# Kernel optimization log

Measured on AMD Instinct MI355X. Metric: run time of the kernel, lower is better.

Reference implementation:

```python
import jax, jax.numpy as jnp
from jax import lax
import numpy as np

NUM_NODES = 30   # pinned by LayerNorm(30) in TCNBlock
H = 4            # heads
C = 64           # channel per head
HC = H * C       # 256 = all_channels, first TCN channel
F_IN = 64
B = 1024         # graphs per batch
EPG = 240        # random edges per graph (no self loops; GATv2 adds them)
LN_EPS = 1e-5
NEG_SLOPE = 0.2


def _glorot(k, shp):
    fan_in = int(np.prod(shp[1:])) if len(shp) > 1 else int(shp[0])
    return jax.random.normal(k, shp, dtype=jnp.float32) / np.sqrt(fan_in)


def setup_inputs():
    key = jax.random.key(0)
    ks = jax.random.split(key, 16)
    N = B * NUM_NODES
    # random intra-graph edges with src != dst (PyG remove_self_loops then add_self_loops)
    src_l = jax.random.randint(ks[0], (B, EPG), 0, NUM_NODES)
    off = jax.random.randint(ks[1], (B, EPG), 1, NUM_NODES)
    dst_l = (src_l + off) % NUM_NODES
    base = (jnp.arange(B) * NUM_NODES)[:, None]
    edge_index = jnp.stack([(src_l + base).reshape(-1), (dst_l + base).reshape(-1)]).astype(jnp.int32)
    z = lambda *s: jnp.zeros(s, jnp.float32)
    return {
        "x": jax.random.normal(ks[2], (N, F_IN), dtype=jnp.float32),
        "gat_Wl": _glorot(ks[3], (HC, F_IN)), "gat_bl": z(HC),
        "gat_Wr": _glorot(ks[4], (HC, F_IN)), "gat_br": z(HC),
        "gat_att": _glorot(ks[5], (H, C)), "gat_bias": z(HC),
        "tcn0_w": _glorot(ks[6], (HC, HC, 3)), "tcn0_b": z(HC),
        "ln0_w": jnp.ones((NUM_NODES,), jnp.float32), "ln0_b": z(NUM_NODES),
        "tcn1_w": _glorot(ks[7], (512, HC, 3)), "tcn1_b": z(512),
        "ln1_w": jnp.ones((NUM_NODES,), jnp.float32), "ln1_b": z(NUM_NODES),
        "ds1_w": _glorot(ks[8], (512, HC, 1)), "ds1_b": z(512),
        "tcn2_w": _glorot(ks[9], (256, 512, 3)), "tcn2_b": z(256),
        "ln2_w": jnp.ones((NUM_NODES,), jnp.float32), "ln2_b": z(NUM_NODES),
        "ds2_w": _glorot(ks[10], (256, 512, 1)), "ds2_b": z(256),
        "fc1_w": _glorot(ks[11], (512, 256 * NUM_NODES)), "fc1_b": z(512),
        "fc2_w": _glorot(ks[12], (256, 512)), "fc2_b": z(256),
        "fc3_w": _glorot(ks[13], (144, 256)), "fc3_b": z(144),
        "edge_index": edge_index,
    }


def _conv1d(x, w, b, dil):
    # torch Conv1d: x [B,Cin,L], w [Cout,Cin,K], padding = dil*(K-1)//2
    pad = dil * (w.shape[-1] - 1) // 2
    y = lax.conv_general_dilated(x, w, (1,), [(pad, pad)], rhs_dilation=(dil,),
                                 dimension_numbers=("NCH", "OIH", "NCH"))
    return y + b[None, :, None]


def _ln(x, w, b):
    # LayerNorm over last dim (length 30)
    mu = jnp.mean(x, -1, keepdims=True)
    var = jnp.var(x, -1, keepdims=True)
    return (x - mu) * lax.rsqrt(var + LN_EPS) * w + b


def reference(x, gat_Wl, gat_bl, gat_Wr, gat_br, gat_att, gat_bias,
              tcn0_w, tcn0_b, ln0_w, ln0_b,
              tcn1_w, tcn1_b, ln1_w, ln1_b, ds1_w, ds1_b,
              tcn2_w, tcn2_b, ln2_w, ln2_b, ds2_w, ds2_b,
              fc1_w, fc1_b, fc2_w, fc2_b, fc3_w, fc3_b, edge_index):
    N = x.shape[0]
    # GATv2Conv default: add self loops
    loops = jnp.arange(N, dtype=edge_index.dtype)
    ei = jnp.concatenate([edge_index, jnp.stack([loops, loops])], axis=1)
    src, dst = ei[0], ei[1]
    xl = (x @ gat_Wl.T + gat_bl).reshape(N, H, C)  # source transform
    xr = (x @ gat_Wr.T + gat_br).reshape(N, H, C)  # target transform
    s = jax.nn.leaky_relu(xl[src] + xr[dst], NEG_SLOPE)          # [E,H,C]
    e = jnp.einsum("ehc,hc->eh", s, gat_att)                     # [E,H]
    m = jax.ops.segment_max(e, dst, num_segments=N)              # segment softmax
    expe = jnp.exp(e - m[dst])
    alpha = expe / jax.ops.segment_sum(expe, dst, num_segments=N)[dst]
    agg = jax.ops.segment_sum(alpha[:, :, None] * xl[src], dst, num_segments=N)
    h = jax.nn.relu(agg.reshape(N, HC) + gat_bias)
    h = h.reshape(-1, NUM_NODES, HC).transpose(0, 2, 1)          # [B, HC, 30]
    # TCN: dilations 1,2,4; residual with 1x1 downsample when channels change
    y = jax.nn.relu(_ln(_conv1d(h, tcn0_w, tcn0_b, 1), ln0_w, ln0_b)) + h
    y = jax.nn.relu(_ln(_conv1d(y, tcn1_w, tcn1_b, 2), ln1_w, ln1_b)) + _conv1d(y, ds1_w, ds1_b, 1)
    y = jax.nn.relu(_ln(_conv1d(y, tcn2_w, tcn2_b, 4), ln2_w, ln2_b)) + _conv1d(y, ds2_w, ds2_b, 1)
    z = y.reshape(y.shape[0], -1)                                # [B, 256*30]
    z = jax.nn.relu(z @ fc1_w.T + fc1_b)
    z = jax.nn.relu(z @ fc2_w.T + fc2_b)
    out = z @ fc3_w.T + fc3_b                                    # [B, 144]
    return out, alpha, ei
```

## Files before the change

### kernel.cpp

```cpp
#include <hip/hip_runtime.h>
#include <hip/hip_bf16.h>

typedef __bf16  bf16x8 __attribute__((ext_vector_type(8)));
typedef __bf16  bf16x4 __attribute__((ext_vector_type(4)));
typedef float   f32x4  __attribute__((ext_vector_type(4)));
typedef __hip_bfloat16 bf;

__device__ __forceinline__ float clamp256(float v) {
    return fminf(fmaxf(v, -256.f), 256.f);
}
__device__ __forceinline__ float sane(float v) {
    return fminf(fmaxf(v, -1e4f), 1e4f);
}
__device__ __forceinline__ int swzk(int k, int col) {
    return (k & ~31) | ((((k >> 3) & 3) ^ ((col >> 1) & 3)) << 3) | (k & 7);
}

template<int TAPS, bool HASWD>
__global__ __launch_bounds__(256) void gemm_tf(
    const bf* __restrict__ A, const bf* __restrict__ Wt, const bf* __restrict__ Wd,
    const float* __restrict__ bias, const float* __restrict__ biasd,
    const float* __restrict__ lnw, const float* __restrict__ lnb,
    const bf* __restrict__ res, int res_stride,
    bf* __restrict__ outb, float* __restrict__ outf, int out_stride,
    int M, int N, int K, int dil, int mode, int relu, int padded, int nn, int kLen)
{
    constexpr int NT = TAPS + (HASWD ? 1 : 0);
    __shared__ __align__(16) unsigned short sA[66 * 40];
    __shared__ __align__(16) unsigned short sB[NT][64 * 40];
    __shared__ float sS[4][64], sS2[4][64];

    const int tid  = threadIdx.x;
    const int wv   = tid >> 6;
    const int lane = tid & 63;
    const int m0   = blockIdx.y * 64;
    const int n0   = blockIdx.x * 64;
    const int frow = lane & 15;
    const int fq   = lane >> 4;
    const int kOff = blockIdx.z * kLen;
    const int kEnd = (kOff + kLen < K) ? (kOff + kLen) : K;

    if (tid < 40) sA[64 * 40 + tid] = (unsigned short)0;

    int aoff[NT];
    {
        int token = wv * 16 + frow;
        int b = token >> 5, l = token & 31;
        #pragma unroll
        for (int t = 0; t < NT; ++t) {
            int s = (t < TAPS) ? (t - TAPS / 2) * dil : 0;
            int ar;
            if (padded) {
                int ls = l + s;
                ar = ((unsigned)ls < 32u) ? (b * 32 + ls) : 64;
            } else {
                ar = token;
            }
            aoff[t] = ar * 40 + fq * 8;
        }
    }

    const int srow = tid >> 2;
    const int schk = (tid & 3) << 3;
    int raG = m0 + srow;
    if (!padded && raG >= M) raG = -1;
    const int rbG  = n0 + srow;
    const bool bval = rbG < N;
    const bf* Ap = (raG >= 0) ? (A + (size_t)raG * K) : nullptr;
    const bf* Bp[NT];
    #pragma unroll
    for (int t = 0; t < NT; ++t)
        Bp[t] = (HASWD && t == TAPS) ? (Wd + (size_t)rbG * K)
                                     : (Wt + ((size_t)t * N + rbG) * K);

    f32x4 accC[4], accR[4];
    #pragma unroll
    for (int i = 0; i < 4; ++i) { accC[i] = 0.f; accR[i] = 0.f; }

    const uint4 zu = make_uint4(0u, 0u, 0u, 0u);
    uint4 pa, pb[NT];
    pa = Ap ? *(const uint4*)(Ap + kOff + schk) : zu;
    #pragma unroll
    for (int t = 0; t < NT; ++t)
        pb[t] = bval ? *(const uint4*)(Bp[t] + kOff + schk) : zu;

    for (int kb = kOff; kb < kEnd; kb += 32) {
        __syncthreads();
        *(uint4*)(sA + srow * 40 + schk) = pa;
        #pragma unroll
        for (int t = 0; t < NT; ++t)
            *(uint4*)(&sB[t][srow * 40 + schk]) = pb[t];
        __syncthreads();
        int kn = kb + 32;
        if (kn < kEnd) {
            pa = Ap ? *(const uint4*)(Ap + kn + schk) : zu;
            #pragma unroll
            for (int t = 0; t < NT; ++t)
                pb[t] = bval ? *(const uint4*)(Bp[t] + kn + schk) : zu;
        }
        #pragma unroll
        for (int t = 0; t < TAPS; ++t) {
            bf16x8 af = *(const bf16x8*)(sA + aoff[t]);
            #pragma unroll
            for (int nt = 0; nt < 4; ++nt) {
                bf16x8 bg = *(const bf16x8*)(&sB[t][(nt * 16 + frow) * 40 + fq * 8]);
                accC[nt] = __builtin_amdgcn_mfma_f32_16x16x32_bf16(af, bg, accC[nt], 0, 0, 0);
            }
        }
        if constexpr (HASWD) {
            bf16x8 af = *(const bf16x8*)(sA + aoff[TAPS]);
            #pragma unroll
            for (int nt = 0; nt < 4; ++nt) {
                bf16x8 bg = *(const bf16x8*)(&sB[TAPS][(nt * 16 + frow) * 40 + fq * 8]);
                accR[nt] = __builtin_amdgcn_mfma_f32_16x16x32_bf16(af, bg, accR[nt], 0, 0, 0);
            }
        }
    }

    if (mode == 0) {
        #pragma unroll
        for (int nt = 0; nt < 4; ++nt) {
            int col = n0 + nt * 16 + frow;
            if (col >= N) continue;
            float bv = bias ? bias[col] : 0.f;
            #pragma unroll
            for (int r = 0; r < 4; ++r) {
                int row = m0 + wv * 16 + fq * 4 + r;
                if (row >= M) continue;
                float v = accC[nt][r] + bv;
                if (relu) v = fmaxf(v, 0.f);
                if (outb) outb[(size_t)row * out_stride + col] = __float2bfloat16(clamp256(v));
                else      outf[(size_t)row * out_stride + col] = sane(v);
            }
        }
    } else if (mode == 3) {
        bf* po = outb + (size_t)blockIdx.z * M * out_stride;
        #pragma unroll
        for (int nt = 0; nt < 4; ++nt) {
            int col = n0 + nt * 16 + frow;
            if (col >= N) continue;
            #pragma unroll
            for (int r = 0; r < 4; ++r) {
                int row = m0 + wv * 16 + fq * 4 + r;
                if (row >= M) continue;
                po[(size_t)row * out_stride + col] = __float2bfloat16(accC[nt][r]);
            }
        }
    } else if (mode == 5) {
        if constexpr (HASWD) {
            bf* out2 = (bf*)res;
            int orow_[4];
            #pragma unroll
            for (int r = 0; r < 4; ++r) {
                int row = m0 + wv * 16 + fq * 4 + r;
                orow_[r] = relu ? ((row / nn) * 32 + (row % nn)) : row;
            }
            #pragma unroll
            for (int nt = 0; nt < 4; ++nt) {
                int col = n0 + nt * 16 + frow;
                if (col >= N) continue;
                float bv = bias[col], bd = biasd[col];
                #pragma unroll
                for (int r = 0; r < 4; ++r) {
                    int row = m0 + wv * 16 + fq * 4 + r;
                    if (row >= M) continue;
                    outb[(size_t)row * out_stride + col] = __float2bfloat16(clamp256(accC[nt][r] + bv));
                    out2[(size_t)orow_[r] * res_stride + col] = __float2bfloat16(clamp256(accR[nt][r] + bd));
                }
            }
        }
    } else {
        float bvc[4], bdc[4];
        #pragma unroll
        for (int nt = 0; nt < 4; ++nt) {
            int col = n0 + nt * 16 + frow;
            bvc[nt] = bias[col];
            bdc[nt] = (HASWD && biasd) ? biasd[col] : 0.f;
        }
        float s[4], s2[4];
        #pragma unroll
        for (int nt = 0; nt < 4; ++nt) { s[nt] = 0.f; s2[nt] = 0.f; }
        #pragma unroll
        for (int nt = 0; nt < 4; ++nt)
            #pragma unroll
            for (int r = 0; r < 4; ++r) {
                int row = wv * 16 + fq * 4 + r;
                int l = row & 31;
                float v = sane(accC[nt][r] + bvc[nt]);
                if (l < nn) { s[nt] += v; s2[nt] += v * v; }
            }
        #pragma unroll
        for (int nt = 0; nt < 4; ++nt) {
            s[nt]  += __shfl_xor(s[nt], 16);  s[nt]  += __shfl_xor(s[nt], 32);
            s2[nt] += __shfl_xor(s2[nt], 16); s2[nt] += __shfl_xor(s2[nt], 32);
        }
        if (fq == 0) {
            #pragma unroll
            for (int nt = 0; nt < 4; ++nt) {
                sS[wv][nt * 16 + frow]  = s[nt];
                sS2[wv][nt * 16 + frow] = s2[nt];
            }
        }
        __syncthreads();
        const int gi = wv >> 1;
        const float inv = 1.f / (float)nn;
        #pragma unroll
        for (int nt = 0; nt < 4; ++nt) {
            int c = nt * 16 + frow;
            int colg = n0 + c;
            float S  = sS[2 * gi][c]  + sS[2 * gi + 1][c];
            float S2 = sS2[2 * gi][c] + sS2[2 * gi + 1][c];
            float mu = S * inv;
            float var = S2 * inv - mu * mu;
            float rs = rsqrtf(fmaxf(var, 0.f) + 1e-5f);
            #pragma unroll
            for (int r = 0; r < 4; ++r) {
                int row = wv * 16 + fq * 4 + r;
                int l = row & 31;
                int grow = m0 + row;
                float outv = 0.f;
                if (l < nn) {
                    float v = (sane(accC[nt][r] + bvc[nt]) - mu) * rs * lnw[l] + lnb[l];
                    v = fmaxf(v, 0.f);
                    float rr;
                    if constexpr (HASWD) rr = sane(accR[nt][r] + bdc[nt]);
                    else rr = __bfloat162float(res[(size_t)grow * res_stride + colg]);
                    outv = clamp256(v + rr);
                }
                outb[(size_t)grow * out_stride + colg] = __float2bfloat16(outv);
            }
        }
    }
}

template<int TAPS, bool HASWD>
__global__ __launch_bounds__(256, 2) void gemm_tcn(
    const bf* __restrict__ A, const bf* __restrict__ Wt, const bf* __restrict__ Wd,
    const float* __restrict__ bias, const float* __restrict__ biasd,
    const float* __restrict__ lnw, const float* __restrict__ lnb,
    const bf* __restrict__ res, int res_stride,
    bf* __restrict__ outb, int out_stride,
    int M, int N, int K, int dil, int nn)
{
    constexpr int NT = TAPS + (HASWD ? 1 : 0);
    constexpr int SA = 257 * 40;
    __shared__ __align__(16) unsigned short sA[2 * SA];
    __shared__ __align__(16) unsigned short sBall[2 * NT * 64 * 32];

    const int tid  = threadIdx.x;
    const int wv   = tid >> 6;
    const int lane = tid & 63;
    const int frow = lane & 15;
    const int fq   = lane >> 4;

    const int gx  = gridDim.x;
    const int nwg = gx * gridDim.y;
    int wg = blockIdx.y * gx + blockIdx.x;
    if ((nwg & 7) == 0) wg = (wg & 7) * (nwg >> 3) + (wg >> 3);
    const int n0 = (wg % gx) * 64;
    const int m0 = (wg / gx) * 256;

    if (tid < 40) {
        sA[256 * 40 + tid]      = (unsigned short)0;
        sA[SA + 256 * 40 + tid] = (unsigned short)0;
    }

    int aoff[TAPS][4];
    #pragma unroll
    for (int mr = 0; mr < 4; ++mr) {
        int token = wv * 64 + mr * 16 + frow;
        int b5 = token >> 5, l = token & 31;
        #pragma unroll
        for (int t = 0; t < TAPS; ++t) {
            int ls = l + (t - TAPS / 2) * dil;
            int ar = ((unsigned)ls < 32u) ? (b5 * 32 + ls) : 256;
            aoff[t][mr] = ar * 40 + fq * 8;
        }
    }
    const int bco = (fq ^ ((frow >> 1) & 3)) << 3;

    const int srow = tid >> 2;
    const int chS  = (tid & 3) << 3;
    const bf* Ap = A + (size_t)(m0 + srow) * K + chS;

    const bf* bsrc[4];
    {
        int lr = lane >> 2, lc = lane & 3;
        #pragma unroll
        for (int i = 0; i < 4; ++i) {
            int colb = n0 + i * 16 + lr;
            const bf* Wb;
            if (HASWD && wv == TAPS) Wb = Wd + (size_t)colb * K;
            else if (wv < TAPS)      Wb = Wt + ((size_t)wv * N + colb) * K;
            else                     Wb = Wt + (size_t)colb * K;
            bsrc[i] = Wb + lc * 8;
        }
    }

    f32x4 accC[4][4], accR[4][4];
    #pragma unroll
    for (int i = 0; i < 4; ++i)
        #pragma unroll
        for (int j = 0; j < 4; ++j) { accC[i][j] = 0.f; if (HASWD) accR[i][j] = 0.f; }

    #define ISSUE_B(BUFB, KBS)                                                      \
        if (wv < NT) {                                                              \
            unsigned short* bas = sBall + ((size_t)((BUFB) * NT + wv) * 64) * 32;   \
            _Pragma("unroll")                                                       \
            for (int i = 0; i < 4; ++i) {                                           \
                __builtin_amdgcn_global_load_lds(                                   \
                    (const __attribute__((address_space(1))) void*)(bsrc[i] + (KBS)), \
                    (__attribute__((address_space(3))) void*)(bas + i * 512),       \
                    16, 0, 0);                                                      \
            }                                                                       \
        }

    uint4 pa[4];
    #pragma unroll
    for (int i = 0; i < 4; ++i) pa[i] = *(const uint4*)(Ap + (size_t)i * 64 * K);
    ISSUE_B(0, 0);
    #pragma unroll
    for (int i = 0; i < 4; ++i)
        *(uint4*)(sA + (srow + i * 64) * 40 + chS) = pa[i];
    __syncthreads();

    int buf = 0;
    for (int kb = 0; kb < K; kb += 32) {
        int kn = kb + 32;
        if (kn < K) {
            #pragma unroll
            for (int i = 0; i < 4; ++i)
                pa[i] = *(const uint4*)(Ap + (size_t)i * 64 * K + kn);
            ISSUE_B(buf ^ 1, kn);
        }
        const unsigned short* sAb = sA + (size_t)buf * SA;
        const unsigned short* sBb = sBall + (size_t)buf * NT * 2048;
        bf16x8 aMid[4];
        #pragma unroll
        for (int mr = 0; mr < 4; ++mr)
            aMid[mr] = *(const bf16x8*)(sAb + aoff[TAPS / 2][mr]);
        #pragma unroll
        for (int t = 0; t < TAPS; ++t) {
            bf16x8 af[4];
            #pragma unroll
            for (int mr = 0; mr < 4; ++mr)
                af[mr] = (t == TAPS / 2) ? aMid[mr]
                                         : *(const bf16x8*)(sAb + aoff[t][mr]);
            #pragma unroll
            for (int nt = 0; nt < 4; ++nt) {
                bf16x8 bg = *(const bf16x8*)(sBb + (size_t)t * 2048 + (nt * 16 + frow) * 32 + bco);
                #pragma unroll
                for (int mr = 0; mr < 4; ++mr)
                    accC[mr][nt] = __builtin_amdgcn_mfma_f32_16x16x32_bf16(af[mr], bg, accC[mr][nt], 0, 0, 0);
            }
        }
        if constexpr (HASWD) {
            #pragma unroll
            for (int nt = 0; nt < 4; ++nt) {
                bf16x8 bg = *(const bf16x8*)(sBb + (size_t)TAPS * 2048 + (nt * 16 + frow) * 32 + bco);
                #pragma unroll
                for (int mr = 0; mr < 4; ++mr)
                    accR[mr][nt] = __builtin_amdgcn_mfma_f32_16x16x32_bf16(aMid[mr], bg, accR[mr][nt], 0, 0, 0);
            }
        }
        if (kn < K) {
            unsigned short* sAn = sA + (size_t)(buf ^ 1) * SA;
            #pragma unroll
            for (int i = 0; i < 4; ++i)
                *(uint4*)(sAn + (srow + i * 64) * 40 + chS) = pa[i];
        }
        __syncthreads();
        buf ^= 1;
    }
    #undef ISSUE_B

    float bvc[4], bdc[4];
    #pragma unroll
    for (int nt = 0; nt < 4; ++nt) {
        int col = n0 + nt * 16 + frow;
        bvc[nt] = bias[col];
        bdc[nt] = HASWD ? biasd[col] : 0.f;
    }
    float S[2][4], Q[2][4];
    #pragma unroll
    for (int h = 0; h < 2; ++h)
        #pragma unroll
        for (int nt = 0; nt < 4; ++nt) { S[h][nt] = 0.f; Q[h][nt] = 0.f; }
    #pragma unroll
    for (int mr = 0; mr < 4; ++mr) {
        const int h = mr >> 1;
        #pragma unroll
        for (int nt = 0; nt < 4; ++nt)
            #pragma unroll
            for (int r = 0; r < 4; ++r) {
                int l = (mr & 1) * 16 + fq * 4 + r;
                if (l < nn) {
                    float v = sane(accC[mr][nt][r] + bvc[nt]);
                    S[h][nt] += v; Q[h][nt] += v * v;
                }
            }
    }
    const float inv = 1.f / (float)nn;
    float mu[2][4], rsg[2][4];
    #pragma unroll
    for (int h = 0; h < 2; ++h)
        #pragma unroll
        for (int nt = 0; nt < 4; ++nt) {
            float s = S[h][nt], q = Q[h][nt];
            s += __shfl_xor(s, 16); s += __shfl_xor(s, 32);
            q += __shfl_xor(q, 16); q += __shfl_xor(q, 32);
            float m = s * inv;
            float var = q * inv - m * m;
            mu[h][nt]  = m;
            rsg[h][nt] = rsqrtf(fmaxf(var, 0.f) + 1e-5f);
        }
    float lw[2][4], lb2[2][4];
    #pragma unroll
    for (int p = 0; p < 2; ++p)
        #pragma unroll
        for (int r = 0; r < 4; ++r) {
            int l = p * 16 + fq * 4 + r;
            bool ok = l < nn;
            lw[p][r]  = ok ? lnw[l] : 0.f;
            lb2[p][r] = ok ? lnb[l] : 0.f;
        }
    #pragma unroll
    for (int nt = 0; nt < 4; ++nt) {
        const int colg = n0 + nt * 16 + frow;
        #pragma unroll
        for (int mr = 0; mr < 4; ++mr) {
            const int h = mr >> 1, p = mr & 1;
            #pragma unroll
            for (int r = 0; r < 4; ++r) {
                int l = p * 16 + fq * 4 + r;
                int grow = m0 + wv * 64 + mr * 16 + fq * 4 + r;
                float outv = 0.f;
                if (l < nn) {
                    float v = (sane(accC[mr][nt][r] + bvc[nt]) - mu[h][nt]) * rsg[h][nt] * lw[p][r] + lb2[p][r];
                    v = fmaxf(v, 0.f);
                    float rr;
                    if constexpr (HASWD) rr = sane(accR[mr][nt][r] + bdc[nt]);
                    else rr = __bfloat162float(res[(size_t)grow * res_stride + colg]);
                    outv = clamp256(v + rr);
                }
                outb[(size_t)grow * out_stride + colg] = __float2bfloat16(outv);
            }
        }
    }
}

#define MAXNE 270
#define XLS   260
#define SHP   264
template<int CONV>
__global__ __launch_bounds__(256, 4) void gat_fused4(
    const int* __restrict__ ei, const bf* __restrict__ xlb, const bf* __restrict__ xrb,
    const float* __restrict__ att, const float* __restrict__ gbias,
    const bf* __restrict__ Wf, const float* __restrict__ cbias,
    const float* __restrict__ lnw, const float* __restrict__ lnb,
    bf* __restrict__ yout, float* __restrict__ dalpha, float* __restrict__ dei,
    int E0, int ET, int EPG, int nn)
{
    __shared__ __align__(16) __bf16 sXL[32 * XLS];
    __shared__ __align__(16) __bf16 sHX[33 * SHP];
    __shared__ float sExp[MAXNE * 4];
    __shared__ int   sSD[MAXNE];
    __shared__ unsigned short sList[MAXNE];
    __shared__ int   sCnt[32];
    __shared__ int   sOff[33];

    const int g = blockIdx.x, tid = threadIdx.x, wv = tid >> 6, lane = tid & 63;
    if (EPG + nn > MAXNE) return;
    const int NE = EPG + nn;

    for (int k = tid; k < EPG; k += 256) {
        int s = ei[(size_t)g * EPG + k] - g * nn;
        int d = ei[(size_t)E0 + (size_t)g * EPG + k] - g * nn;
        s = min(max(s, 0), nn - 1);
        d = min(max(d, 0), nn - 1);
        sSD[k] = s | (d << 16);
    }
    for (int k = EPG + tid; k < NE; k += 256) {
        int node = k - EPG;
        sSD[k] = node | (node << 16);
    }
    {
        const uint4* gxl = (const uint4*)(xlb + (size_t)g * nn * 256);
        const uint4* gxr = (const uint4*)(xrb + (size_t)g * (CONV ? 32 : nn) * 256);
        for (int k = tid; k < nn * 32; k += 256) {
            int node = k >> 5, c8 = k & 31;
            *(uint4*)(sXL + node * XLS + c8 * 8) = gxl[k];
            *(uint4*)(sHX + k * 8) = gxr[k];
        }
    }
    if (CONV) { __bf16 z = (__bf16)0.f; for (int k = tid; k < SHP; k += 256) sHX[32 * SHP + k] = z; }
    if (tid < 32) sCnt[tid] = 0;
    __syncthreads();

    for (int k = tid; k < NE; k += 256) atomicAdd(&sCnt[sSD[k] >> 16], 1);
    __syncthreads();
    if (tid < 32) {
        int acc = 0, last = 0;
        #pragma unroll
        for (int j = 0; j < 32; ++j) {
            int c = sCnt[j];
            if (j < tid) acc += c;
            if (j == 31) last = c;
        }
        sOff[tid] = acc;
        if (tid == 31) sOff[32] = acc + last;
        sCnt[tid] = 0;
    }
    __syncthreads();
    for (int k = tid; k < NE; k += 256) {
        int d = sSD[k] >> 16;
        int p = atomicAdd(&sCnt[d], 1);
        sList[sOff[d] + p] = (unsigned short)k;
    }

    for (int k = tid; k < NE; k += 256) {
        int s, d; size_t eg;
        if (k < EPG) {
            int sd = sSD[k];
            s = g * nn + (sd & 0xffff); d = g * nn + (sd >> 16);
            eg = (size_t)g * EPG + k;
        }
        else { int node = g * nn + (k - EPG); s = d = node; eg = (size_t)E0 + (size_t)g * nn + (k - EPG); }
        dei[eg] = (float)s;
        dei[(size_t)ET + eg] = (float)d;
    }
    __syncthreads();

    const float4 attv = *(const float4*)(att + lane * 4);
    const int h4 = lane >> 4;
    for (int i = wv; i < NE; i += 4) {
        int sd = sSD[i];
        int srcl = sd & 0xffff, dstl = sd >> 16;
        bf16x4 a = *(const bf16x4*)(sXL + srcl * XLS + lane * 4);
        bf16x4 b = *(const bf16x4*)(sHX + dstl * 256 + lane * 4);
        float p = 0.f;
        {
            float v0 = (float)a[0] + (float)b[0]; v0 = v0 > 0.f ? v0 : 0.2f * v0; p += v0 * attv.x;
            float v1 = (float)a[1] + (float)b[1]; v1 = v1 > 0.f ? v1 : 0.2f * v1; p += v1 * attv.y;
            float v2 = (float)a[2] + (float)b[2]; v2 = v2 > 0.f ? v2 : 0.2f * v2; p += v2 * attv.z;
            float v3 = (float)a[3] + (float)b[3]; v3 = v3 > 0.f ? v3 : 0.2f * v3; p += v3 * attv.w;
        }
        p += __shfl_xor(p, 1); p += __shfl_xor(p, 2);
        p += __shfl_xor(p, 4); p += __shfl_xor(p, 8);
        if ((lane & 15) == 0)
            sExp[i * 4 + h4] = __expf(fminf(fmaxf(p, -60.f), 60.f));
    }
    __syncthreads();

    {
        const int grp  = wv * 8 + (lane >> 3);
        const int s8   = lane & 7;
        const int chb  = s8 * 32;
        const int head = s8 >> 1;
        bf* hrow = yout + ((size_t)g * 32 + grp) * 256 + chb;

        if (grp < nn) {
            const int beg = sOff[grp], end = sOff[grp + 1];
            float den = 0.f;
            f32x4 acc[8];
            #pragma unroll
            for (int k2 = 0; k2 < 8; ++k2) acc[k2] = 0.f;

            for (int q = beg; q < end; ++q) {
                int e = sList[q];
                float ev = sExp[e * 4 + head];
                den += ev;
                const __bf16* xp = sXL + (sSD[e] & 0xffff) * XLS + chb;
                #pragma unroll
                for (int k2 = 0; k2 < 4; ++k2) {
                    bf16x8 xa = *(const bf16x8*)(xp + k2 * 8);
                    #pragma unroll
                    for (int j = 0; j < 4; ++j)
                        acc[k2 * 2][j]     += ev * (float)xa[j];
                    #pragma unroll
                    for (int j = 0; j < 4; ++j)
                        acc[k2 * 2 + 1][j] += ev * (float)xa[4 + j];
                }
            }
            const float rden = 1.f / fmaxf(den, 1e-30f);

            if (!(s8 & 1)) {
                for (int q = beg; q < end; ++q) {
                    int e = sList[q];
                    float al = fminf(fmaxf(sExp[e * 4 + head] * rden, 0.f), 1.f);
                    size_t eg = (e < EPG) ? ((size_t)g * EPG + e)
                                          : ((size_t)E0 + (size_t)g * nn + (e - EPG));
                    dalpha[eg * 4 + head] = al;
                }
            }

            #pragma unroll
            for (int k2 = 0; k2 < 8; ++k2) {
                float4 gbv = *(const float4*)(gbias + chb + k2 * 4);
                bf16x4 o;
                o[0] = (__bf16)clamp256(fmaxf(acc[k2][0] * rden + gbv.x, 0.f));
                o[1] = (__bf16)clamp256(fmaxf(acc[k2][1] * rden + gbv.y, 0.f));
                o[2] = (__bf16)clamp256(fmaxf(acc[k2][2] * rden + gbv.z, 0.f));
                o[3] = (__bf16)clamp256(fmaxf(acc[k2][3] * rden + gbv.w, 0.f));
                if constexpr (CONV) *(bf16x4*)(sHX + grp * SHP + chb + k2 * 4) = o;
                else                *(bf16x4*)(hrow + k2 * 4) = o;
            }
        } else {
            bf16x4 z; z[0] = (__bf16)0.f; z[1] = (__bf16)0.f; z[2] = (__bf16)0.f; z[3] = (__bf16)0.f;
            #pragma unroll
            for (int k2 = 0; k2 < 8; ++k2) {
                if constexpr (CONV) *(bf16x4*)(sHX + grp * SHP + chb + k2 * 4) = z;
                else                *(bf16x4*)(hrow + k2 * 4) = z;
            }
        }
    }

    if constexpr (CONV) {
        __syncthreads();
        const int frow = lane & 15;
        const int fq   = lane >> 4;
        const int colw = wv * 64;
        f32x4 c0[2][4];
        #pragma unroll
        for (int i = 0; i < 2; ++i)
            #pragma unroll
            for (int j = 0; j < 4; ++j) c0[i][j] = 0.f;

        #pragma unroll
        for (int kc = 0; kc < 8; ++kc) {
            bf16x8 af[3][2];
            #pragma unroll
            for (int t = 0; t < 3; ++t)
                #pragma unroll
                for (int mr = 0; mr < 2; ++mr) {
                    int l = mr * 16 + frow + t - 1;
                    int ar = ((unsigned)l < 32u) ? l : 32;
                    af[t][mr] = *(const bf16x8*)(sHX + ar * SHP + kc * 32 + fq * 8);
                }
            #pragma unroll
            for (int t = 0; t < 3; ++t) {
                bf16x8 bgs[4];
                #pragma unroll
                for (int nt = 0; nt < 4; ++nt) {
                    const __bf16* bp = (const __bf16*)Wf +
                        ((((size_t)(t * 16 + (colw >> 4) + nt) * 8 + kc) * 16 + frow) * 4 + fq) * 8;
                    bgs[nt] = *(const bf16x8*)bp;
                }
                #pragma unroll
                for (int nt = 0; nt < 4; ++nt) {
                    c0[0][nt] = __builtin_amdgcn_mfma_f32_16x16x32_bf16(af[t][0], bgs[nt], c0[0][nt], 0, 0, 0);
                    c0[1][nt] = __builtin_amdgcn_mfma_f32_16x16x32_bf16(af[t][1], bgs[nt], c0[1][nt], 0, 0, 0);
                }
            }
        }

        float bv[4];
        #pragma unroll
        for (int nt = 0; nt < 4; ++nt) bv[nt] = cbias[colw + nt * 16 + frow];
        float S[4], Q[4];
        #pragma unroll
        for (int nt = 0; nt < 4; ++nt) { S[nt] = 0.f; Q[nt] = 0.f; }
        #pragma unroll
        for (int mr = 0; mr < 2; ++mr)
            #pragma unroll
            for (int nt = 0; nt < 4; ++nt)
                #pragma unroll
                for (int r = 0; r < 4; ++r) {
                    int l = mr * 16 + fq * 4 + r;
                    if (l < nn) {
                        float v = sane(c0[mr][nt][r] + bv[nt]);
                        S[nt] += v; Q[nt] += v * v;
                    }
                }
        const float inv = 1.f / (float)nn;
        float mu[4], rsg[4];
        #pragma unroll
        for (int nt = 0; nt < 4; ++nt) {
            float s = S[nt], q = Q[nt];
            s += __shfl_xor(s, 16); s += __shfl_xor(s, 32);
            q += __shfl_xor(q, 16); q += __shfl_xor(q, 32);
            float m = s * inv;
            float var = q * inv - m * m;
            mu[nt]  = m;
            rsg[nt] = rsqrtf(fmaxf(var, 0.f) + 1e-5f);
        }
        float lw[2][4], lb2[2][4];
        #pragma unroll
        for (int p = 0; p < 2; ++p)
            #pragma unroll
            for (int r = 0; r < 4; ++r) {
                int l = p * 16 + fq * 4 + r;
                bool ok = l < nn;
                lw[p][r]  = ok ? lnw[l] : 0.f;
                lb2[p][r] = ok ? lnb[l] : 0.f;
            }
        #pragma unroll
        for (int nt = 0; nt < 4; ++nt) {
            const int colf = colw + nt * 16 + frow;
            #pragma unroll
            for (int mr = 0; mr < 2; ++mr)
                #pragma unroll
                for (int r = 0; r < 4; ++r) {
                    int l = mr * 16 + fq * 4 + r;
                    float outv = 0.f;
                    if (l < nn) {
                        float v = (sane(c0[mr][nt][r] + bv[nt]) - mu[nt]) * rsg[nt] * lw[mr][r] + lb2[mr][r];
                        v = fmaxf(v, 0.f);
                        float rr = (float)sHX[l * SHP + colf];
                        outv = clamp256(v + rr);
                    }
                    yout[((size_t)g * 32 + l) * 256 + colf] = __float2bfloat16(outv);
                }
        }
    }
}

struct CvtSegs { const float* in[7]; bf* out[7]; int n[7]; };
__global__ void prep_cvt(CvtSegs s, int total)
{
    int idx = blockIdx.x * 256 + threadIdx.x;
    if (idx >= total) return;
    #pragma unroll
    for (int i = 0; i < 7; ++i) {
        if (idx < s.n[i]) { s.out[i][idx] = __float2bfloat16(s.in[i][idx]); return; }
        idx -= s.n[i];
    }
}
struct TapSegs { const float* w[3]; bf* o[3]; int cc[3]; int kk[3]; int swz[3]; };
__global__ void prep_taps3(TapSegs s, int total)
{
    int idx = blockIdx.x * 256 + threadIdx.x;
    if (idx >= total) return;
    #pragma unroll
    for (int i = 0; i < 3; ++i) {
        if (idx < s.cc[i]) {
            unsigned K = (unsigned)s.kk[i];
            unsigned co = (unsigned)idx / K, ci = (unsigned)idx % K;
            int dst = co * K + (s.swz[i] ? swzk(ci, co) : ci);
            #pragma unroll
            for (int k = 0; k < 3; ++k)
                s.o[i][(size_t)k * s.cc[i] + dst] = __float2bfloat16(s.w[i][(size_t)idx * 3 + k]);
            return;
        }
        idx -= s.cc[i];
    }
}
__global__ void prep_wswz(const float* __restrict__ w, bf* __restrict__ o,
                          int total, int K, int swz)
{
    int idx = blockIdx.x * 256 + threadIdx.x;
    if (idx >= total) return;
    int co = idx / K, ci = idx % K;
    o[(size_t)co * K + (swz ? swzk(ci, co) : ci)] = __float2bfloat16(w[idx]);
}
__global__ void prep_bfrag(const float* __restrict__ w, bf* __restrict__ o, int HC)
{
    int idx = blockIdx.x * 256 + threadIdx.x;
    if (idx >= HC * HC) return;
    int co = idx / HC, ci = idx % HC;
    int cg = co >> 4, fr = co & 15, kc = ci >> 5, fq = (ci >> 3) & 3, w8 = ci & 7;
    int NCg = HC >> 4, NKc = HC >> 5;
    #pragma unroll
    for (int t = 0; t < 3; ++t) {
        size_t dst = (((((size_t)t * NCg + cg) * NKc + kc) * 16 + fr) * 4 + fq) * 8 + w8;
        o[dst] = __float2bfloat16(w[(size_t)idx * 3 + t]);
    }
}

__global__ void prep_fc1(const float* __restrict__ w, bf* __restrict__ o, int F1, int nn, int HC)
{
    int idx = blockIdx.x * 256 + threadIdx.x;
    int kw = 32 * HC;
    if (idx >= F1 * kw) return;
    int co = idx / kw, r = idx % kw, l = r / HC, ci = r % HC;
    float hv = 0.f;
    if (l < nn) hv = w[(size_t)co * (HC * nn) + ci * nn + l];
    o[idx] = __float2bfloat16(hv);
}

__global__ void fc1red(const bf* __restrict__ zp, const float* __restrict__ bias,
                       bf* __restrict__ o, int MN, int N, int S)
{
    int idx = blockIdx.x * 256 + threadIdx.x;
    if (idx >= MN) return;
    float s = 0.f;
    for (int z = 0; z < S; ++z) s += __bfloat162float(zp[(size_t)z * MN + idx]);
    o[idx] = __float2bfloat16(clamp256(fmaxf(s + bias[idx % N], 0.f)));
}

extern "C" void kernel_launch(void* const* d_in, const int* in_sizes, int n_in,
                              void* d_out, int out_size, void* d_ws, size_t ws_size,
                              hipStream_t stream)
{
    (void)n_in; (void)ws_size;
    const float* x   = (const float*)d_in[0];
    const float* Wl  = (const float*)d_in[1];  const float* bl  = (const float*)d_in[2];
    const float* Wr  = (const float*)d_in[3];  const float* br  = (const float*)d_in[4];
    const float* att = (const float*)d_in[5];  const float* gb  = (const float*)d_in[6];
    const float* t0w = (const float*)d_in[7];  const float* t0b = (const float*)d_in[8];
    const float* l0w = (const float*)d_in[9];  const float* l0b = (const float*)d_in[10];
    const float* t1w = (const float*)d_in[11]; const float* t1b = (const float*)d_in[12];
    const float* l1w = (const float*)d_in[13]; const float* l1b = (const float*)d_in[14];
    const float* d1w = (const float*)d_in[15]; const float* d1b = (const float*)d_in[16];
    const float* t2w = (const float*)d_in[17]; const float* t2b = (const float*)d_in[18];
    const float* l2w = (const float*)d_in[19]; const float* l2b = (const float*)d_in[20];
    const float* d2w = (const float*)d_in[21]; const float* d2b = (const float*)d_in[22];
    const float* f1w = (const float*)d_in[23]; const float* f1b = (const float*)d_in[24];
    const float* f2w = (const float*)d_in[25]; const float* f2b = (const float*)d_in[26];
    const float* f3w = (const float*)d_in[27]; const float* f3b = (const float*)d_in[28];
    const int*   ei  = (const int*)d_in[29];

    const int HC   = in_sizes[6];
    const int F_IN = in_sizes[1] / (HC > 0 ? HC : 1);
    const int NN   = in_sizes[0] / (F_IN > 0 ? F_IN : 1);
    const int E0   = in_sizes[29] / 2;
    const int ET   = E0 + NN;
    int nn = in_sizes[9];  nn = nn < 1 ? 1 : (nn > 32 ? 32 : nn);
    const int NG   = NN / nn;
    const int EPG  = NG > 0 ? E0 / NG : 0;
    const int C1   = in_sizes[12];
    const int C2   = in_sizes[18];
    const int F1   = in_sizes[24];
    const int F2   = in_sizes[26];
    const int F3   = in_sizes[28];
    const int NG2  = (NG + 1) / 2;

    float* dout   = (float*)d_out;
    float* dei    = dout + ((size_t)out_size - 2 * (size_t)ET);
    float* dalpha = dei - (size_t)ET * 4;

    const bool fused0 = (HC == 256) && (nn >= 1) && (nn <= 32) && (EPG + nn <= MAXNE)
                        && ((NN % 64) == 0);
    const int  gcA = NG2, gcB = NG - NG2;
    const bool fastc = ((gcA * 32) % 256 == 0) && ((gcB * 32) % 256 == 0)
                       && (C1 % 64 == 0) && (C2 % 64 == 0)
                       && (HC % 32 == 0) && (C1 % 32 == 0);

    char* ws = (char*)d_ws;
    const size_t MB = 1ull << 20;
    bf*    xb   = (bf*)(ws);
    bf*    WkA  = (bf*)(ws + 4 * MB);
    bf*    WkB  = WkA + (size_t)3 * HC * HC;
    bf*    WkC  = WkB + (size_t)3 * C1 * HC;
    bf*    Wlb  = WkC + (size_t)3 * C2 * C1;
    bf*    Wrb  = Wlb + (size_t)HC * F_IN;
    bf*    f2wb = Wrb + (size_t)HC * F_IN;
    bf*    f3wb = f2wb + (size_t)F2 * F1;
    bf*    d1wb = f3wb + (size_t)F3 * F2;
    bf*    d2wb = d1wb + (size_t)C1 * HC;
    bf*    WkAf = d2wb + (size_t)C2 * C1;
    char*  S0   = ws + (size_t)(7.5 * MB);
    char*  S1   = ws + 25 * MB;

    bf*    xrb  = (bf*)S0;
    bf*    hbuf = (bf*)S0;
    bf*    xlb  = (bf*)S1;
    bf*    y0   = fused0 ? (bf*)S0 : (bf*)S1;
    bf*    y1c  = fused0 ? (bf*)S1 : (bf*)S0;
    char*  fcS  = fused0 ? S1 : S0;
    bf*    W1t  = (bf*)fcS;
    bf*    z1p  = (bf*)(fcS + (size_t)(8.5 * MB));
    bf*    z1   = (bf*)(ws);
    bf*    z2   = (bf*)(ws + 2 * MB);

    {
        CvtSegs cs;
        cs.in[0] = x;   cs.out[0] = xb;   cs.n[0] = NN * F_IN;
        cs.in[1] = Wl;  cs.out[1] = Wlb;  cs.n[1] = HC * F_IN;
        cs.in[2] = Wr;  cs.out[2] = Wrb;  cs.n[2] = HC * F_IN;
        cs.in[3] = f2w; cs.out[3] = f2wb; cs.n[3] = F2 * F1;
        cs.in[4] = f3w; cs.out[4] = f3wb; cs.n[4] = F3 * F2;
        cs.in[5] = nullptr; cs.out[5] = nullptr; cs.n[5] = 0;
        cs.in[6] = nullptr; cs.out[6] = nullptr; cs.n[6] = 0;
        int tot = 0; for (int i = 0; i < 5; ++i) tot += cs.n[i];
        prep_cvt<<<(tot + 255) / 256, 256, 0, stream>>>(cs, tot);
        TapSegs ts;
        ts.w[0] = t0w; ts.o[0] = WkA; ts.cc[0] = HC * HC; ts.kk[0] = HC; ts.swz[0] = 0;
        ts.w[1] = t1w; ts.o[1] = WkB; ts.cc[1] = C1 * HC; ts.kk[1] = HC; ts.swz[1] = fastc ? 1 : 0;
        ts.w[2] = t2w; ts.o[2] = WkC; ts.cc[2] = C2 * C1; ts.kk[2] = C1; ts.swz[2] = fastc ? 1 : 0;
        int tt = ts.cc[0] + ts.cc[1] + ts.cc[2];
        prep_taps3<<<(tt + 255) / 256, 256, 0, stream>>>(ts, tt);
        prep_wswz<<<(C1 * HC + 255) / 256, 256, 0, stream>>>(d1w, d1wb, C1 * HC, HC, fastc ? 1 : 0);
        prep_wswz<<<(C2 * C1 + 255) / 256, 256, 0, stream>>>(d2w, d2wb, C2 * C1, C1, fastc ? 1 : 0);
        if (fused0)
            prep_bfrag<<<(HC * HC + 255) / 256, 256, 0, stream>>>(t0w, WkAf, HC);
    }

    gemm_tf<1, true><<<dim3((HC + 63) / 64, (NN + 63) / 64), 256, 0, stream>>>(
        xb, Wlb, Wrb, bl, br, nullptr, nullptr, (const bf*)xrb, HC,
        xlb, nullptr, HC, NN, HC, F_IN, 1, 5, fused0 ? 1 : 0, 0, nn, F_IN);

    if (fused0)
        gat_fused4<1><<<NG, 256, 0, stream>>>(ei, xlb, xrb, att, gb,
                                              WkAf, t0b, l0w, l0b,
                                              y0, dalpha, dei, E0, ET, EPG, nn);
    else {
        gat_fused4<0><<<NG, 256, 0, stream>>>(ei, xlb, xrb, att, gb,
                                              nullptr, nullptr, nullptr, nullptr,
                                              hbuf, dalpha, dei, E0, ET, EPG, nn);
        gemm_tf<3, false><<<dim3((HC + 63) / 64, NG * 32 / 64), 256, 0, stream>>>(
            hbuf, WkA, nullptr, t0b, nullptr, l0w, l0b, hbuf, HC,
            y0, nullptr, HC, NG * 32, HC, HC, 1, 2, 0, 1, nn, HC);
    }

    for (int c = 0; c < 2; ++c) {
        int g0 = c * NG2;
        int gc = (c == 0) ? NG2 : (NG - NG2);
        if (gc <= 0) continue;
        const bf* y0c = y0 + (size_t)g0 * 32 * HC;
        bf*       y2c = y0 + (size_t)g0 * 32 * HC;
        if (fastc) {
            gemm_tcn<3, true><<<dim3(C1 / 64, gc * 32 / 256), 256, 0, stream>>>(
                y0c, WkB, d1wb, t1b, d1b, l1w, l1b, nullptr, 0,
                y1c, C1, gc * 32, C1, HC, 2, nn);
            gemm_tcn<3, true><<<dim3(C2 / 64, gc * 32 / 256), 256, 0, stream>>>(
                y1c, WkC, d2wb, t2b, d2b, l2w, l2b, nullptr, 0,
                y2c, C2, gc * 32, C2, C1, 4, nn);
        } else {
            gemm_tf<3, true><<<dim3((C1 + 63) / 64, gc * 32 / 64), 256, 0, stream>>>(
                y0c, WkB, d1wb, t1b, d1b, l1w, l1b, nullptr, 0,
                y1c, nullptr, C1, gc * 32, C1, HC, 2, 2, 0, 1, nn, HC);
            gemm_tf<3, true><<<dim3((C2 + 63) / 64, gc * 32 / 64), 256, 0, stream>>>(
                y1c, WkC, d2wb, t2b, d2b, l2w, l2b, nullptr, 0,
                y2c, nullptr, C2, gc * 32, C2, C1, 4, 2, 0, 1, nn, C1);
        }
    }

    prep_fc1<<<(F1 * 32 * HC + 255) / 256, 256, 0, stream>>>(f1w, W1t, F1, nn, HC);
    gemm_tf<1, false><<<dim3((F1 + 63) / 64, (NG + 63) / 64, 8), 256, 0, stream>>>(
        y0, W1t, nullptr, nullptr, nullptr, nullptr, nullptr, nullptr, 0,
        z1p, nullptr, F1, NG, F1, 32 * HC, 1, 3, 0, 0, nn, 4 * HC);
    fc1red<<<(NG * F1 + 255) / 256, 256, 0, stream>>>(z1p, f1b, z1, NG * F1, F1, 8);

    gemm_tf<1, false><<<dim3((F2 + 63) / 64, (NG + 63) / 64), 256, 0, stream>>>(
        z1, f2wb, nullptr, f2b, nullptr, nullptr, nullptr, nullptr, 0,
        z2, nullptr, F2, NG, F2, F1, 1, 0, 1, 0, nn, F1);
    gemm_tf<1, false><<<dim3((F3 + 63) / 64, (NG + 63) / 64), 256, 0, stream>>>(
        z2, f3wb, nullptr, f3b, nullptr, nullptr, nullptr, nullptr, 0,
        nullptr, dout, F3, NG, F3, F2, 1, 0, 0, 0, nn, F2);
}
```

Before: 454.4 us.

## Fuse GATv2 left/right linear projections into the per-graph GAT kernel

The separate gemm_tf launch that computed xl and xr for all nodes is removed on the fused path. Each per-graph GAT block now loads the raw bf16 node features into shared memory (reusing the sExp buffer) and computes both projections with MFMA, using weights pre-packed into fragment layout by a new prep kernel. This avoids writing the xl/xr intermediates to global memory and reading them back, and saves one launch. In exchange the GAT kernel does more work, carries more register pressure, and each block re-reads the projection weights from global memory.

```diff
diff --git a/kernel.cpp b/kernel.cpp
--- a/kernel.cpp
+++ b/kernel.cpp
@@ -455,6 +455,7 @@
 template<int CONV>
 __global__ __launch_bounds__(256, 4) void gat_fused4(
     const int* __restrict__ ei, const bf* __restrict__ xlb, const bf* __restrict__ xrb,
+    const bf* __restrict__ Wlr, const float* __restrict__ gbl, const float* __restrict__ gbr,
     const float* __restrict__ att, const float* __restrict__ gbias,
     const bf* __restrict__ Wf, const float* __restrict__ cbias,
     const float* __restrict__ lnw, const float* __restrict__ lnb,
@@ -463,7 +464,7 @@
 {
     __shared__ __align__(16) __bf16 sXL[32 * XLS];
     __shared__ __align__(16) __bf16 sHX[33 * SHP];
-    __shared__ float sExp[MAXNE * 4];
+    __shared__ __align__(16) float sExp[MAXNE * 4];
     __shared__ int   sSD[MAXNE];
     __shared__ unsigned short sList[MAXNE];
     __shared__ int   sCnt[32];
@@ -472,6 +473,8 @@
     const int g = blockIdx.x, tid = threadIdx.x, wv = tid >> 6, lane = tid & 63;
     if (EPG + nn > MAXNE) return;
     const int NE = EPG + nn;
+    const int frow = lane & 15;
+    const int fq   = lane >> 4;
 
     for (int k = tid; k < EPG; k += 256) {
         int s = ei[(size_t)g * EPG + k] - g * nn;
@@ -484,20 +487,78 @@
         int node = k - EPG;
         sSD[k] = node | (node << 16);
     }
-    {
+    if constexpr (CONV) {
+        unsigned short* sXg = (unsigned short*)sExp;
+        const uint4* gx = (const uint4*)(xlb + (size_t)g * nn * 64);
+        for (int k = tid; k < nn * 8; k += 256) {
+            int node = k >> 3, k8 = k & 7;
+            *(uint4*)(sXg + node * 64 + ((k8 ^ (node & 7)) << 3)) = gx[k];
+        }
+        const uint4 zu = make_uint4(0u, 0u, 0u, 0u);
+        for (int k = nn * 8 + tid; k < 32 * 8; k += 256) {
+            int node = k >> 3, k8 = k & 7;
+            *(uint4*)(sXg + node * 64 + ((k8 ^ (node & 7)) << 3)) = zu;
+        }
+        __bf16 z = (__bf16)0.f;
+        for (int k = tid; k < SHP; k += 256) sHX[32 * SHP + k] = z;
+    } else {
         const uint4* gxl = (const uint4*)(xlb + (size_t)g * nn * 256);
-        const uint4* gxr = (const uint4*)(xrb + (size_t)g * (CONV ? 32 : nn) * 256);
+        const uint4* gxr = (const uint4*)(xrb + (size_t)g * nn * 256);
         for (int k = tid; k < nn * 32; k += 256) {
             int node = k >> 5, c8 = k & 31;
             *(uint4*)(sXL + node * XLS + c8 * 8) = gxl[k];
-            *(uint4*)(sHX + k * 8) = gxr[k];
-        }
-    }
-    if (CONV) { __bf16 z = (__bf16)0.f; for (int k = tid; k < SHP; k += 256) sHX[32 * SHP + k] = z; }
+            *(uint4*)(sHX + node * SHP + c8 * 8) = gxr[k];
+        }
+    }
     if (tid < 32) sCnt[tid] = 0;
     __syncthreads();
 
     for (int k = tid; k < NE; k += 256) atomicAdd(&sCnt[sSD[k] >> 16], 1);
+    if constexpr (CONV) {
+        const unsigned short* sXg = (const unsigned short*)sExp;
+        bf16x8 axf[2][2];
+        #pragma unroll
+        for (int mr = 0; mr < 2; ++mr)
+            #pragma unroll
+            for (int kc = 0; kc < 2; ++kc) {
+                int row = mr * 16 + frow;
+                axf[mr][kc] = *(const bf16x8*)(sXg + row * 64 + (((kc * 4 + fq) ^ (row & 7)) << 3));
+            }
+        const int colw = wv * 64;
+        #pragma unroll
+        for (int out = 0; out < 2; ++out) {
+            f32x4 ga[2][4];
+            #pragma unroll
+            for (int mr = 0; mr < 2; ++mr)
+                #pragma unroll
+                for (int ct = 0; ct < 4; ++ct) ga[mr][ct] = 0.f;
+            #pragma unroll
+            for (int kc = 0; kc < 2; ++kc)
+                #pragma unroll
+                for (int ct = 0; ct < 4; ++ct) {
+                    const __bf16* bp = (const __bf16*)Wlr + (size_t)out * 16384 +
+                        ((((size_t)(((colw >> 4) + ct) * 2 + kc) * 16 + frow) * 4 + fq) * 8);
+                    bf16x8 bg = *(const bf16x8*)bp;
+                    ga[0][ct] = __builtin_amdgcn_mfma_f32_16x16x32_bf16(axf[0][kc], bg, ga[0][ct], 0, 0, 0);
+                    ga[1][ct] = __builtin_amdgcn_mfma_f32_16x16x32_bf16(axf[1][kc], bg, ga[1][ct], 0, 0, 0);
+                }
+            const float* bb = out ? gbr : gbl;
+            #pragma unroll
+            for (int ct = 0; ct < 4; ++ct) {
+                int col = colw + ct * 16 + frow;
+                float b = bb[col];
+                #pragma unroll
+                for (int mr = 0; mr < 2; ++mr)
+                    #pragma unroll
+                    for (int r = 0; r < 4; ++r) {
+                        int row = mr * 16 + fq * 4 + r;
+                        float v = clamp256(ga[mr][ct][r] + b);
+                        if (out == 0) sXL[row * XLS + col] = (__bf16)v;
+                        else          sHX[row * SHP + col] = (__bf16)v;
+                    }
+            }
+        }
+    }
     __syncthreads();
     if (tid < 32) {
         int acc = 0, last = 0;
@@ -537,7 +598,7 @@
         int sd = sSD[i];
         int srcl = sd & 0xffff, dstl = sd >> 16;
         bf16x4 a = *(const bf16x4*)(sXL + srcl * XLS + lane * 4);
-        bf16x4 b = *(const bf16x4*)(sHX + dstl * 256 + lane * 4);
+        bf16x4 b = *(const bf16x4*)(sHX + dstl * SHP + lane * 4);
         float p = 0.f;
         {
             float v0 = (float)a[0] + (float)b[0]; v0 = v0 > 0.f ? v0 : 0.2f * v0; p += v0 * attv.x;
@@ -617,8 +678,6 @@
 
     if constexpr (CONV) {
         __syncthreads();
-        const int frow = lane & 15;
-        const int fq   = lane >> 4;
         const int colw = wv * 64;
         f32x4 c0[2][4];
         #pragma unroll
@@ -765,6 +824,20 @@
         size_t dst = (((((size_t)t * NCg + cg) * NKc + kc) * 16 + fr) * 4 + fq) * 8 + w8;
         o[dst] = __float2bfloat16(w[(size_t)idx * 3 + t]);
     }
+}
+__global__ void prep_gwfrag(const float* __restrict__ wl, const float* __restrict__ wr,
+                            bf* __restrict__ o, int HC, int FI)
+{
+    int idx = blockIdx.x * 256 + threadIdx.x;
+    int tot = HC * FI;
+    if (idx >= 2 * tot) return;
+    const float* w = (idx < tot) ? wl : wr;
+    int j = (idx < tot) ? idx : idx - tot;
+    int col = j / FI, k = j % FI;
+    int cg = col >> 4, fr = col & 15, kc = k >> 5, fq = (k >> 3) & 3, w8 = k & 7;
+    size_t dst = (size_t)((idx < tot) ? 0 : 1) * tot +
+        ((((size_t)(cg * (FI >> 5) + kc) * 16 + fr) * 4 + fq) * 8 + w8);
+    o[dst] = __float2bfloat16(w[j]);
 }
 
 __global__ void prep_fc1(const float* __restrict__ w, bf* __restrict__ o, int F1, int nn, int HC)
@@ -829,8 +902,8 @@
     float* dei    = dout + ((size_t)out_size - 2 * (size_t)ET);
     float* dalpha = dei - (size_t)ET * 4;
 
-    const bool fused0 = (HC == 256) && (nn >= 1) && (nn <= 32) && (EPG + nn <= MAXNE)
-                        && ((NN % 64) == 0);
+    const bool fused0 = (HC == 256) && (F_IN == 64) && (nn >= 1) && (nn <= 32)
+                        && (EPG + nn <= MAXNE) && ((NN % 64) == 0);
     const int  gcA = NG2, gcB = NG - NG2;
     const bool fastc = ((gcA * 32) % 256 == 0) && ((gcB * 32) % 256 == 0)
                        && (C1 % 64 == 0) && (C2 % 64 == 0)
@@ -849,6 +922,7 @@
     bf*    d1wb = f3wb + (size_t)F3 * F2;
     bf*    d2wb = d1wb + (size_t)C1 * HC;
     bf*    WkAf = d2wb + (size_t)C2 * C1;
+    bf*    WlrF = WkAf + (size_t)3 * HC * HC;
     char*  S0   = ws + (size_t)(7.5 * MB);
     char*  S1   = ws + 25 * MB;
 
@@ -882,21 +956,22 @@
         prep_taps3<<<(tt + 255) / 256, 256, 0, stream>>>(ts, tt);
         prep_wswz<<<(C1 * HC + 255) / 256, 256, 0, stream>>>(d1w, d1wb, C1 * HC, HC, fastc ? 1 : 0);
         prep_wswz<<<(C2 * C1 + 255) / 256, 256, 0, stream>>>(d2w, d2wb, C2 * C1, C1, fastc ? 1 : 0);
-        if (fused0)
+        if (fused0) {
             prep_bfrag<<<(HC * HC + 255) / 256, 256, 0, stream>>>(t0w, WkAf, HC);
-    }
-
-    gemm_tf<1, true><<<dim3((HC + 63) / 64, (NN + 63) / 64), 256, 0, stream>>>(
-        xb, Wlb, Wrb, bl, br, nullptr, nullptr, (const bf*)xrb, HC,
-        xlb, nullptr, HC, NN, HC, F_IN, 1, 5, fused0 ? 1 : 0, 0, nn, F_IN);
-
-    if (fused0)
-        gat_fused4<1><<<NG, 256, 0, stream>>>(ei, xlb, xrb, att, gb,
-                                              WkAf, t0b, l0w, l0b,
+            prep_gwfrag<<<(2 * HC * F_IN + 255) / 256, 256, 0, stream>>>(Wl, Wr, WlrF, HC, F_IN);
+        }
+    }
+
+    if (fused0) {
+        gat_fused4<1><<<NG, 256, 0, stream>>>(ei, xb, nullptr, WlrF, bl, br,
+                                              att, gb, WkAf, t0b, l0w, l0b,
                                               y0, dalpha, dei, E0, ET, EPG, nn);
-    else {
-        gat_fused4<0><<<NG, 256, 0, stream>>>(ei, xlb, xrb, att, gb,
-                                              nullptr, nullptr, nullptr, nullptr,
+    } else {
+        gemm_tf<1, true><<<dim3((HC + 63) / 64, (NN + 63) / 64), 256, 0, stream>>>(
+            xb, Wlb, Wrb, bl, br, nullptr, nullptr, (const bf*)xrb, HC,
+            xlb, nullptr, HC, NN, HC, F_IN, 1, 5, 0, 0, nn, F_IN);
+        gat_fused4<0><<<NG, 256, 0, stream>>>(ei, xlb, xrb, nullptr, nullptr, nullptr,
+                                              att, gb, nullptr, nullptr, nullptr, nullptr,
                                               hbuf, dalpha, dei, E0, ET, EPG, nn);
         gemm_tf<3, false><<<dim3((HC + 63) / 64, NG * 32 / 64), 256, 0, stream>>>(
             hbuf, WkA, nullptr, t0b, nullptr, l0w, l0b, hbuf, HC,
```

Result: faster. 424.0 us (-6.7%).
